# Performance work log

Hardware: AMD Instinct MI355X
Metric: run time of the kernel (lower is better)

Reference implementation:

```python
import jax, jax.numpy as jnp
import numpy as np


def setup_inputs() -> dict:
    key = jax.random.key(0)
    k0, k1, k2, k3, k4 = jax.random.split(key, 5)
    T, B, S, H = 32, 8192, 256, 128
    return {
        "states_batch": jax.random.normal(k0, (T, B, S), dtype=jnp.float32),
        "W1": jax.random.normal(k1, (T, S, H), dtype=jnp.float32) * (S ** -0.5),
        "b1": jax.random.normal(k2, (T, H), dtype=jnp.float32) * 0.01,
        "W2": jax.random.normal(k3, (T, H, 1), dtype=jnp.float32) * 0.01,
        "b2": jax.random.normal(k4, (T, 1), dtype=jnp.float32) * 0.01,
    }


def reference(states_batch, W1, b1, W2, b2):
    # [T,B,S] @ [T,S,H] -> [T,B,H], bias, SiLU
    h = jnp.einsum('tbs,tsh->tbh', states_batch, W1) + b1[:, None, :]
    h = jax.nn.silu(h)
    # [T,B,H] @ [T,H,1] -> [T,B,1], bias, squeeze -> [T,B]
    out = jnp.einsum('tbh,tho->tbo', h, W2) + b2[:, None, :]
    return out.squeeze(-1)
```

## Files before the change

### kernel.cpp

```cpp
#include <hip/hip_runtime.h>
#include <hip/hip_bf16.h>

typedef __attribute__((ext_vector_type(8))) short bf16x8;
typedef __attribute__((ext_vector_type(4))) float f32x4;

#define T_DIM 32
#define B_DIM 8192
#define S_DIM 256
#define H_DIM 128
#define BM    64
#define NCHUNK (B_DIM / BM)

__device__ __forceinline__ uint32_t cvt_pk_bf16(float lo, float hi) {
  uint32_t r;
  asm("v_cvt_pk_bf16_f32 %0, %1, %2" : "=v"(r) : "v"(lo), "v"(hi));
  return r;
}

__global__ __launch_bounds__(256, 2) void cvar_mlp_kernel(
    const float* __restrict__ states, const float* __restrict__ W1,
    const float* __restrict__ b1, const float* __restrict__ W2,
    const float* __restrict__ b2, float* __restrict__ out)
{
  __shared__ __align__(16) char lds[BM * 512];
  __shared__ float red[4][BM];

  const int tid  = threadIdx.x;
  const int wid  = tid >> 6;
  const int lane = tid & 63;
  const int l15  = lane & 15;
  const int lg   = lane >> 4;

  const int bidx   = blockIdx.x;
  const int xcd    = bidx & 7;
  const int slot   = bidx >> 3;
  const int t      = xcd * 4 + (slot >> 7);
  const int bchunk = slot & 127;
  const int b0     = bchunk * BM;

  const float*  Ag  = states + ((size_t)t * B_DIM + b0) * S_DIM;
  const float*  W1g = W1 + (size_t)t * (S_DIM * H_DIM);
  const float4* A4  = reinterpret_cast<const float4*>(Ag);

  float4 av[16];
#pragma unroll
  for (int i = 0; i < 16; ++i)
    av[i] = A4[i * 256 + tid];

  bf16x8 bfr[2][8];
#pragma unroll
  for (int nloc = 0; nloc < 2; ++nloc) {
    const int ncol = (wid * 2 + nloc) * 16 + l15;
#pragma unroll
    for (int ks = 0; ks < 8; ++ks) {
      const int kbase = ks * 32 + lg * 8;
      float e[8];
#pragma unroll
      for (int j = 0; j < 8; ++j)
        e[j] = W1g[(size_t)(kbase + j) * H_DIM + ncol];
      union { uint32_t u[4]; bf16x8 v; } uu;
      uu.u[0] = cvt_pk_bf16(e[0], e[1]);
      uu.u[1] = cvt_pk_bf16(e[2], e[3]);
      uu.u[2] = cvt_pk_bf16(e[4], e[5]);
      uu.u[3] = cvt_pk_bf16(e[6], e[7]);
      bfr[nloc][ks] = uu.v;
    }
  }

#pragma unroll
  for (int i = 0; i < 16; ++i) {
    const int f   = i * 256 + tid;
    const int row = f >> 6;
    const int kq  = f & 63;
    const uint32_t lo = cvt_pk_bf16(av[i].x, av[i].y);
    const uint32_t hi = cvt_pk_bf16(av[i].z, av[i].w);
    int byteoff = row * 512 + kq * 8;
    byteoff ^= (row & 7) << 4;
    *reinterpret_cast<uint2*>(&lds[byteoff]) = make_uint2(lo, hi);
  }
  __syncthreads();

  f32x4 acc[4][2];
#pragma unroll
  for (int mt = 0; mt < 4; ++mt)
#pragma unroll
    for (int nloc = 0; nloc < 2; ++nloc)
      acc[mt][nloc] = (f32x4){0.f, 0.f, 0.f, 0.f};

#pragma unroll
  for (int mt = 0; mt < 4; ++mt) {
    const int row = mt * 16 + l15;
    bf16x8 afr[8];
#pragma unroll
    for (int ks = 0; ks < 8; ++ks) {
      int byteoff = row * 512 + ks * 64 + lg * 16;
      byteoff ^= (row & 7) << 4;
      afr[ks] = *reinterpret_cast<const bf16x8*>(&lds[byteoff]);
    }
#pragma unroll
    for (int ks = 0; ks < 8; ++ks) {
      acc[mt][0] = __builtin_amdgcn_mfma_f32_16x16x32_bf16(afr[ks], bfr[0][ks], acc[mt][0], 0, 0, 0);
      acc[mt][1] = __builtin_amdgcn_mfma_f32_16x16x32_bf16(afr[ks], bfr[1][ks], acc[mt][1], 0, 0, 0);
    }
  }

  float b1c[2], w2c[2];
#pragma unroll
  for (int nloc = 0; nloc < 2; ++nloc) {
    const int col = (wid * 2 + nloc) * 16 + l15;
    b1c[nloc] = b1[(size_t)t * H_DIM + col];
    w2c[nloc] = W2[(size_t)t * H_DIM + col];
  }

#pragma unroll
  for (int mt = 0; mt < 4; ++mt) {
    float part[4];
#pragma unroll
    for (int r = 0; r < 4; ++r) {
      float s = 0.f;
#pragma unroll
      for (int nloc = 0; nloc < 2; ++nloc) {
        const float h   = acc[mt][nloc][r] + b1c[nloc];
        const float sig = 1.f / (1.f + __expf(-h));
        s += h * sig * w2c[nloc];
      }
      s += __shfl_xor(s, 1);
      s += __shfl_xor(s, 2);
      s += __shfl_xor(s, 4);
      s += __shfl_xor(s, 8);
      part[r] = s;
    }
    if (l15 == 0) {
#pragma unroll
      for (int r = 0; r < 4; ++r)
        red[wid][mt * 16 + lg * 4 + r] = part[r];
    }
  }
  __syncthreads();

  if (tid < BM) {
    const float o = red[0][tid] + red[1][tid] + red[2][tid] + red[3][tid] + b2[t];
    out[(size_t)t * B_DIM + b0 + tid] = o;
  }
}

extern "C" void kernel_launch(void* const* d_in, const int* in_sizes, int n_in,
                              void* d_out, int out_size, void* d_ws, size_t ws_size,
                              hipStream_t stream) {
  const float* states = (const float*)d_in[0];
  const float* W1     = (const float*)d_in[1];
  const float* b1     = (const float*)d_in[2];
  const float* W2     = (const float*)d_in[3];
  const float* b2     = (const float*)d_in[4];
  float* out          = (float*)d_out;

  const int grid = T_DIM * NCHUNK;
  cvar_mlp_kernel<<<grid, 256, 0, stream>>>(states, W1, b1, W2, b2, out);
}
```

Before: 65.20 us.

## Process four row chunks per block with double-buffered LDS prefetch

Each block now handles four 64-row chunks of the batch instead of one, so the W1 fragment load and bf16 conversion is amortized across chunks. The next chunk's states are prefetched into registers during the current chunk's MFMA work and written into an alternate LDS buffer. This cuts the grid by four and reduces redundant weight traffic, at the cost of fewer blocks for latency hiding and doubled LDS usage.

```diff
diff --git a/kernel.cpp b/kernel.cpp
--- a/kernel.cpp
+++ b/kernel.cpp
@@ -9,7 +9,8 @@
 #define S_DIM 256
 #define H_DIM 128
 #define BM    64
-#define NCHUNK (B_DIM / BM)
+#define NCH   4
+#define BLOCKS_PER_T 32
 
 __device__ __forceinline__ uint32_t cvt_pk_bf16(float lo, float hi) {
   uint32_t r;
@@ -22,8 +23,8 @@
     const float* __restrict__ b1, const float* __restrict__ W2,
     const float* __restrict__ b2, float* __restrict__ out)
 {
-  __shared__ __align__(16) char lds[BM * 512];
-  __shared__ float red[4][BM];
+  __shared__ __align__(16) char lds[2][BM * 512];
+  __shared__ float red[2][4][BM];
 
   const int tid  = threadIdx.x;
   const int wid  = tid >> 6;
@@ -31,16 +32,16 @@
   const int l15  = lane & 15;
   const int lg   = lane >> 4;
 
-  const int bidx   = blockIdx.x;
-  const int xcd    = bidx & 7;
-  const int slot   = bidx >> 3;
-  const int t      = xcd * 4 + (slot >> 7);
-  const int bchunk = slot & 127;
-  const int b0     = bchunk * BM;
+  const int bidx = blockIdx.x;
+  const int xcd  = bidx & 7;
+  const int slot = bidx >> 3;
+  const int t    = xcd * 4 + (slot >> 5);
+  const int cg   = slot & 31;
+  const int b0   = cg * (BM * NCH);
 
   const float*  Ag  = states + ((size_t)t * B_DIM + b0) * S_DIM;
+  const float4* A4  = reinterpret_cast<const float4*>(Ag);
   const float*  W1g = W1 + (size_t)t * (S_DIM * H_DIM);
-  const float4* A4  = reinterpret_cast<const float4*>(Ag);
 
   float4 av[16];
 #pragma unroll
@@ -67,6 +68,16 @@
     }
   }
 
+  float b1c[2], w2c[2];
+#pragma unroll
+  for (int nloc = 0; nloc < 2; ++nloc) {
+    const int col = (wid * 2 + nloc) * 16 + l15;
+    b1c[nloc] = b1[(size_t)t * H_DIM + col];
+    w2c[nloc] = W2[(size_t)t * H_DIM + col];
+  }
+  const float b2t = b2[t];
+  float* outt = out + (size_t)t * B_DIM + b0;
+
 #pragma unroll
   for (int i = 0; i < 16; ++i) {
     const int f   = i * 256 + tid;
@@ -76,71 +87,88 @@
     const uint32_t hi = cvt_pk_bf16(av[i].z, av[i].w);
     int byteoff = row * 512 + kq * 8;
     byteoff ^= (row & 7) << 4;
-    *reinterpret_cast<uint2*>(&lds[byteoff]) = make_uint2(lo, hi);
+    *reinterpret_cast<uint2*>(&lds[0][byteoff]) = make_uint2(lo, hi);
   }
   __syncthreads();
 
-  f32x4 acc[4][2];
+  for (int c = 0; c < NCH; ++c) {
+    const int cur = c & 1;
+
+    if (c + 1 < NCH) {
 #pragma unroll
-  for (int mt = 0; mt < 4; ++mt)
+      for (int i = 0; i < 16; ++i)
+        av[i] = A4[(c + 1) * (BM * S_DIM / 4) + i * 256 + tid];
+    }
+
+    f32x4 acc[4][2];
 #pragma unroll
-    for (int nloc = 0; nloc < 2; ++nloc)
-      acc[mt][nloc] = (f32x4){0.f, 0.f, 0.f, 0.f};
+    for (int mt = 0; mt < 4; ++mt)
+#pragma unroll
+      for (int nloc = 0; nloc < 2; ++nloc)
+        acc[mt][nloc] = (f32x4){0.f, 0.f, 0.f, 0.f};
 
 #pragma unroll
-  for (int mt = 0; mt < 4; ++mt) {
-    const int row = mt * 16 + l15;
-    bf16x8 afr[8];
+    for (int mt = 0; mt < 4; ++mt) {
+      const int row = mt * 16 + l15;
+      bf16x8 afr[8];
 #pragma unroll
-    for (int ks = 0; ks < 8; ++ks) {
-      int byteoff = row * 512 + ks * 64 + lg * 16;
-      byteoff ^= (row & 7) << 4;
-      afr[ks] = *reinterpret_cast<const bf16x8*>(&lds[byteoff]);
+      for (int ks = 0; ks < 8; ++ks) {
+        int byteoff = row * 512 + ks * 64 + lg * 16;
+        byteoff ^= (row & 7) << 4;
+        afr[ks] = *reinterpret_cast<const bf16x8*>(&lds[cur][byteoff]);
+      }
+#pragma unroll
+      for (int ks = 0; ks < 8; ++ks) {
+        acc[mt][0] = __builtin_amdgcn_mfma_f32_16x16x32_bf16(afr[ks], bfr[0][ks], acc[mt][0], 0, 0, 0);
+        acc[mt][1] = __builtin_amdgcn_mfma_f32_16x16x32_bf16(afr[ks], bfr[1][ks], acc[mt][1], 0, 0, 0);
+      }
     }
-#pragma unroll
-    for (int ks = 0; ks < 8; ++ks) {
-      acc[mt][0] = __builtin_amdgcn_mfma_f32_16x16x32_bf16(afr[ks], bfr[0][ks], acc[mt][0], 0, 0, 0);
-      acc[mt][1] = __builtin_amdgcn_mfma_f32_16x16x32_bf16(afr[ks], bfr[1][ks], acc[mt][1], 0, 0, 0);
-    }
-  }
-
-  float b1c[2], w2c[2];
-#pragma unroll
-  for (int nloc = 0; nloc < 2; ++nloc) {
-    const int col = (wid * 2 + nloc) * 16 + l15;
-    b1c[nloc] = b1[(size_t)t * H_DIM + col];
-    w2c[nloc] = W2[(size_t)t * H_DIM + col];
-  }
 
 #pragma unroll
-  for (int mt = 0; mt < 4; ++mt) {
-    float part[4];
+    for (int mt = 0; mt < 4; ++mt) {
+      float part[4];
 #pragma unroll
-    for (int r = 0; r < 4; ++r) {
-      float s = 0.f;
+      for (int r = 0; r < 4; ++r) {
+        float s = 0.f;
 #pragma unroll
-      for (int nloc = 0; nloc < 2; ++nloc) {
-        const float h   = acc[mt][nloc][r] + b1c[nloc];
-        const float sig = 1.f / (1.f + __expf(-h));
-        s += h * sig * w2c[nloc];
+        for (int nloc = 0; nloc < 2; ++nloc) {
+          const float h   = acc[mt][nloc][r] + b1c[nloc];
+          const float sig = 1.f / (1.f + __expf(-h));
+          s += h * sig * w2c[nloc];
+        }
+        s += __shfl_xor(s, 1);
+        s += __shfl_xor(s, 2);
+        s += __shfl_xor(s, 4);
+        s += __shfl_xor(s, 8);
+        part[r] = s;
       }
-      s += __shfl_xor(s, 1);
-      s += __shfl_xor(s, 2);
-      s += __shfl_xor(s, 4);
-      s += __shfl_xor(s, 8);
-      part[r] = s;
+      if (l15 == 0) {
+#pragma unroll
+        for (int r = 0; r < 4; ++r)
+          red[cur][wid][mt * 16 + lg * 4 + r] = part[r];
+      }
     }
-    if (l15 == 0) {
+
+    if (c + 1 < NCH) {
 #pragma unroll
-      for (int r = 0; r < 4; ++r)
-        red[wid][mt * 16 + lg * 4 + r] = part[r];
+      for (int i = 0; i < 16; ++i) {
+        const int f   = i * 256 + tid;
+        const int row = f >> 6;
+        const int kq  = f & 63;
+        const uint32_t lo = cvt_pk_bf16(av[i].x, av[i].y);
+        const uint32_t hi = cvt_pk_bf16(av[i].z, av[i].w);
+        int byteoff = row * 512 + kq * 8;
+        byteoff ^= (row & 7) << 4;
+        *reinterpret_cast<uint2*>(&lds[cur ^ 1][byteoff]) = make_uint2(lo, hi);
+      }
     }
-  }
-  __syncthreads();
+    __syncthreads();
 
-  if (tid < BM) {
-    const float o = red[0][tid] + red[1][tid] + red[2][tid] + red[3][tid] + b2[t];
-    out[(size_t)t * B_DIM + b0 + tid] = o;
+    if (tid < BM) {
+      const float o = red[cur][0][tid] + red[cur][1][tid] +
+                      red[cur][2][tid] + red[cur][3][tid] + b2t;
+      outt[c * BM + tid] = o;
+    }
   }
 }
 
@@ -154,6 +182,6 @@
   const float* b2     = (const float*)d_in[4];
   float* out          = (float*)d_out;
 
-  const int grid = T_DIM * NCHUNK;
+  const int grid = T_DIM * BLOCKS_PER_T;
   cvar_mlp_kernel<<<grid, 256, 0, stream>>>(states, W1, b1, W2, b2, out);
 }
```

Measured after the change: 58.64 us. 1.11x faster.

## Stage W1 in LDS once per block and stream row chunks with register double buffering

Applied to the files above, without the earlier changes.

Each block now covers 512 rows of one task instead of 64, so W1 is converted to bf16 into LDS once and reused across 8 chunks per wave. States are loaded straight into MFMA A-fragment registers with ping-pong buffers, removing the A staging through LDS and the cross-wave reduction. Each wave computes all 128 hidden columns itself and writes its outputs directly. This trades per-block parallelism (far fewer blocks, 64KB LDS) for much less redundant W1 traffic and overlapped loads.

```diff
diff --git a/kernel.cpp b/kernel.cpp
--- a/kernel.cpp
+++ b/kernel.cpp
@@ -8,8 +8,8 @@
 #define B_DIM 8192
 #define S_DIM 256
 #define H_DIM 128
-#define BM    64
-#define NCHUNK (B_DIM / BM)
+#define NCH   8
+#define BLOCKS_PER_T 16
 
 __device__ __forceinline__ uint32_t cvt_pk_bf16(float lo, float hi) {
   uint32_t r;
@@ -17,13 +17,61 @@
   return r;
 }
 
+#define ISSUE(av, c)                                                           \
+  _Pragma("unroll")                                                            \
+  for (int ks = 0; ks < 8; ++ks) {                                             \
+    av[ks * 2]     = A4[(c) * 1024 + l15 * 64 + ks * 8 + lg * 2];              \
+    av[ks * 2 + 1] = A4[(c) * 1024 + l15 * 64 + ks * 8 + lg * 2 + 1];          \
+  }
+
+#define COMPUTE(av, c)                                                         \
+  {                                                                            \
+    f32x4 acc[8];                                                              \
+    _Pragma("unroll")                                                          \
+    for (int nt = 0; nt < 8; ++nt) acc[nt] = (f32x4){0.f, 0.f, 0.f, 0.f};      \
+    _Pragma("unroll")                                                          \
+    for (int ks = 0; ks < 8; ++ks) {                                           \
+      union { uint32_t u[4]; bf16x8 v; } uu;                                   \
+      uu.u[0] = cvt_pk_bf16(av[ks * 2].x,     av[ks * 2].y);                   \
+      uu.u[1] = cvt_pk_bf16(av[ks * 2].z,     av[ks * 2].w);                   \
+      uu.u[2] = cvt_pk_bf16(av[ks * 2 + 1].x, av[ks * 2 + 1].y);               \
+      uu.u[3] = cvt_pk_bf16(av[ks * 2 + 1].z, av[ks * 2 + 1].w);               \
+      _Pragma("unroll")                                                        \
+      for (int nt = 0; nt < 8; ++nt) {                                         \
+        const bf16x8 bq = *reinterpret_cast<const bf16x8*>(                    \
+            &ldsW[((nt * 8 + ks) * 64 + lane) * 16]);                          \
+        acc[nt] = __builtin_amdgcn_mfma_f32_16x16x32_bf16(uu.v, bq,            \
+                                                          acc[nt], 0, 0, 0);  \
+      }                                                                        \
+    }                                                                          \
+    float part[4];                                                             \
+    _Pragma("unroll")                                                          \
+    for (int r = 0; r < 4; ++r) {                                              \
+      float s = 0.f;                                                           \
+      _Pragma("unroll")                                                        \
+      for (int nt = 0; nt < 8; ++nt) {                                         \
+        const float h   = acc[nt][r] + b1c[nt];                                \
+        const float sig = 1.f / (1.f + __expf(-h));                            \
+        s += h * sig * w2c[nt];                                                \
+      }                                                                        \
+      s += __shfl_xor(s, 1);                                                   \
+      s += __shfl_xor(s, 2);                                                   \
+      s += __shfl_xor(s, 4);                                                   \
+      s += __shfl_xor(s, 8);                                                   \
+      part[r] = s;                                                             \
+    }                                                                          \
+    if (l15 == 0) {                                                            \
+      f32x4 o = {part[0] + b2t, part[1] + b2t, part[2] + b2t, part[3] + b2t};  \
+      *reinterpret_cast<f32x4*>(&outw[(c) * 16 + lg * 4]) = o;                 \
+    }                                                                          \
+  }
+
 __global__ __launch_bounds__(256, 2) void cvar_mlp_kernel(
     const float* __restrict__ states, const float* __restrict__ W1,
     const float* __restrict__ b1, const float* __restrict__ W2,
     const float* __restrict__ b2, float* __restrict__ out)
 {
-  __shared__ __align__(16) char lds[BM * 512];
-  __shared__ float red[4][BM];
+  __shared__ __align__(16) char ldsW[64 * 1024];
 
   const int tid  = threadIdx.x;
   const int wid  = tid >> 6;
@@ -31,26 +79,24 @@
   const int l15  = lane & 15;
   const int lg   = lane >> 4;
 
-  const int bidx   = blockIdx.x;
-  const int xcd    = bidx & 7;
-  const int slot   = bidx >> 3;
-  const int t      = xcd * 4 + (slot >> 7);
-  const int bchunk = slot & 127;
-  const int b0     = bchunk * BM;
+  const int bidx = blockIdx.x;
+  const int xcd  = bidx & 7;
+  const int slot = bidx >> 3;
+  const int t    = xcd * 4 + (slot >> 4);
+  const int cg   = slot & 15;
 
-  const float*  Ag  = states + ((size_t)t * B_DIM + b0) * S_DIM;
-  const float*  W1g = W1 + (size_t)t * (S_DIM * H_DIM);
-  const float4* A4  = reinterpret_cast<const float4*>(Ag);
+  const float*  Aw = states + ((size_t)t * B_DIM + cg * 512 + wid * 128) * S_DIM;
+  const float4* A4 = reinterpret_cast<const float4*>(Aw);
+  float*       outw = out + (size_t)t * B_DIM + cg * 512 + wid * 128;
 
-  float4 av[16];
+  float4 avA[16], avB[16];
+  ISSUE(avA, 0);
+
+  const float* W1g = W1 + (size_t)t * (S_DIM * H_DIM);
 #pragma unroll
-  for (int i = 0; i < 16; ++i)
-    av[i] = A4[i * 256 + tid];
-
-  bf16x8 bfr[2][8];
-#pragma unroll
-  for (int nloc = 0; nloc < 2; ++nloc) {
-    const int ncol = (wid * 2 + nloc) * 16 + l15;
+  for (int p = 0; p < 2; ++p) {
+    const int nt   = wid * 2 + p;
+    const int ncol = nt * 16 + l15;
 #pragma unroll
     for (int ks = 0; ks < 8; ++ks) {
       const int kbase = ks * 32 + lg * 8;
@@ -63,84 +109,27 @@
       uu.u[1] = cvt_pk_bf16(e[2], e[3]);
       uu.u[2] = cvt_pk_bf16(e[4], e[5]);
       uu.u[3] = cvt_pk_bf16(e[6], e[7]);
-      bfr[nloc][ks] = uu.v;
+      *reinterpret_cast<bf16x8*>(&ldsW[((nt * 8 + ks) * 64 + lane) * 16]) = uu.v;
     }
   }
 
+  float b1c[8], w2c[8];
 #pragma unroll
-  for (int i = 0; i < 16; ++i) {
-    const int f   = i * 256 + tid;
-    const int row = f >> 6;
-    const int kq  = f & 63;
-    const uint32_t lo = cvt_pk_bf16(av[i].x, av[i].y);
-    const uint32_t hi = cvt_pk_bf16(av[i].z, av[i].w);
-    int byteoff = row * 512 + kq * 8;
-    byteoff ^= (row & 7) << 4;
-    *reinterpret_cast<uint2*>(&lds[byteoff]) = make_uint2(lo, hi);
+  for (int nt = 0; nt < 8; ++nt) {
+    const int col = nt * 16 + l15;
+    b1c[nt] = b1[(size_t)t * H_DIM + col];
+    w2c[nt] = W2[(size_t)t * H_DIM + col];
   }
+  const float b2t = b2[t];
+
   __syncthreads();
 
-  f32x4 acc[4][2];
-#pragma unroll
-  for (int mt = 0; mt < 4; ++mt)
-#pragma unroll
-    for (int nloc = 0; nloc < 2; ++nloc)
-      acc[mt][nloc] = (f32x4){0.f, 0.f, 0.f, 0.f};
-
-#pragma unroll
-  for (int mt = 0; mt < 4; ++mt) {
-    const int row = mt * 16 + l15;
-    bf16x8 afr[8];
-#pragma unroll
-    for (int ks = 0; ks < 8; ++ks) {
-      int byteoff = row * 512 + ks * 64 + lg * 16;
-      byteoff ^= (row & 7) << 4;
-      afr[ks] = *reinterpret_cast<const bf16x8*>(&lds[byteoff]);
-    }
-#pragma unroll
-    for (int ks = 0; ks < 8; ++ks) {
-      acc[mt][0] = __builtin_amdgcn_mfma_f32_16x16x32_bf16(afr[ks], bfr[0][ks], acc[mt][0], 0, 0, 0);
-      acc[mt][1] = __builtin_amdgcn_mfma_f32_16x16x32_bf16(afr[ks], bfr[1][ks], acc[mt][1], 0, 0, 0);
-    }
-  }
-
-  float b1c[2], w2c[2];
-#pragma unroll
-  for (int nloc = 0; nloc < 2; ++nloc) {
-    const int col = (wid * 2 + nloc) * 16 + l15;
-    b1c[nloc] = b1[(size_t)t * H_DIM + col];
-    w2c[nloc] = W2[(size_t)t * H_DIM + col];
-  }
-
-#pragma unroll
-  for (int mt = 0; mt < 4; ++mt) {
-    float part[4];
-#pragma unroll
-    for (int r = 0; r < 4; ++r) {
-      float s = 0.f;
-#pragma unroll
-      for (int nloc = 0; nloc < 2; ++nloc) {
-        const float h   = acc[mt][nloc][r] + b1c[nloc];
-        const float sig = 1.f / (1.f + __expf(-h));
-        s += h * sig * w2c[nloc];
-      }
-      s += __shfl_xor(s, 1);
-      s += __shfl_xor(s, 2);
-      s += __shfl_xor(s, 4);
-      s += __shfl_xor(s, 8);
-      part[r] = s;
-    }
-    if (l15 == 0) {
-#pragma unroll
-      for (int r = 0; r < 4; ++r)
-        red[wid][mt * 16 + lg * 4 + r] = part[r];
-    }
-  }
-  __syncthreads();
-
-  if (tid < BM) {
-    const float o = red[0][tid] + red[1][tid] + red[2][tid] + red[3][tid] + b2[t];
-    out[(size_t)t * B_DIM + b0 + tid] = o;
+#pragma unroll 1
+  for (int c = 0; c < NCH; c += 2) {
+    ISSUE(avB, c + 1);
+    COMPUTE(avA, c);
+    if (c + 2 < NCH) { ISSUE(avA, c + 2); }
+    COMPUTE(avB, c + 1);
   }
 }
 
@@ -154,6 +143,6 @@
   const float* b2     = (const float*)d_in[4];
   float* out          = (float*)d_out;
 
-  const int grid = T_DIM * NCHUNK;
+  const int grid = T_DIM * BLOCKS_PER_T;
   cvar_mlp_kernel<<<grid, 256, 0, stream>>>(states, W1, b1, W2, b2, out);
 }
```

New measurement: 57.93 us. -11.2%, faster.
